# Kernel optimization log

Hardware: AMD Instinct MI355X
Metric: run time of the kernel (lower is better)

The kernel has to match this reference:

```python
import jax, jax.numpy as jnp
import numpy as np

EPS = 1e-05
DILATION = 1

def setup_inputs() -> dict:
    key = jax.random.key(0)
    k1, k2 = jax.random.split(key)
    B, T, D, K = 4, 4096, 2048, 4
    x = jax.random.normal(k1, (B, T, D), dtype=jnp.float32)
    norm_weight = jnp.ones((D,), dtype=jnp.float32)
    conv_weight = jax.random.normal(k2, (D, 1, K), dtype=jnp.float32) * (1.0 / np.sqrt(K))
    return {"x": x, "norm_weight": norm_weight, "conv_weight": conv_weight}

def reference(x, norm_weight, conv_weight):
    B, T, D = x.shape
    K = conv_weight.shape[-1]
    pad = (K - 1) * DILATION
    # RMSNorm over last dim
    ms = jnp.mean(jnp.square(x), axis=-1, keepdims=True)
    y = x * jax.lax.rsqrt(ms + EPS) * norm_weight
    # to channel-first [B, D, T]
    y = jnp.transpose(y, (0, 2, 1))
    # causal depthwise conv: left-pad (K-1)*dilation, valid conv == torch pad-both + slice[:T]
    y = jax.lax.conv_general_dilated(
        y, conv_weight,
        window_strides=(1,),
        padding=[(pad, 0)],
        rhs_dilation=(DILATION,),
        dimension_numbers=("NCH", "OIH", "NCH"),
        feature_group_count=D,
    )
    # SiLU then back to [B, T, D]
    y = y * jax.nn.sigmoid(y)
    return jnp.transpose(y, (0, 2, 1))
```

## Files before the change

kernel.cpp:

```cpp
#include <hip/hip_runtime.h>
#include <math.h>

#define D_DIM 2048
#define T_DIM 4096
#define TT    16
#define NT    (D_DIM / 4)
#define NW    (NT / 64)

typedef float vfloat4 __attribute__((ext_vector_type(4)));

__device__ __forceinline__ float row_partial(float4 v) {
    float p = v.x * v.x + v.y * v.y + v.z * v.z + v.w * v.w;
#pragma unroll
    for (int off = 32; off > 0; off >>= 1) p += __shfl_down(p, off, 64);
    return p;
}

__device__ __forceinline__ float inv_from(const float* sp) {
    float4 a = *(const float4*)sp;
    float4 b = *(const float4*)(sp + 4);
    float s = a.x + a.y + a.z + a.w + b.x + b.y + b.z + b.w;
    return rsqrtf(s * (1.0f / D_DIM) + 1e-5f);
}

__device__ __forceinline__ float silu(float v) {
    return v * __builtin_amdgcn_rcpf(1.f + __expf(-v));
}

__device__ __forceinline__ void nt_store4(float* p, float a, float b, float c, float d) {
    vfloat4 v = { a, b, c, d };
    __builtin_nontemporal_store(v, (vfloat4*)p);
}

__global__ __launch_bounds__(NT, 4) void fused_kernel(
    const float* __restrict__ x,
    const float* __restrict__ g,
    const float* __restrict__ w,
    float* __restrict__ out)
{
    const int b    = blockIdx.y;
    const int t0   = blockIdx.x * TT;
    const int tid  = threadIdx.x;
    const int d0   = tid * 4;
    const int lane = tid & 63;
    const int wid  = tid >> 6;

    __shared__ __align__(16) float part[TT + 3][NW];

    const float* xb = x   + (size_t)b * T_DIM * D_DIM + d0;
    float*       ob = out + (size_t)b * T_DIM * D_DIM + d0;

    float4 hv[3];
#pragma unroll
    for (int r = 0; r < 3; ++r) {
        const int t = t0 - 3 + r;
        hv[r] = (t >= 0) ? *(const float4*)(xb + (size_t)t * D_DIM)
                         : make_float4(0.f, 0.f, 0.f, 0.f);
    }
    float4 xv[TT];
#pragma unroll
    for (int i = 0; i < TT; ++i)
        xv[i] = *(const float4*)(xb + (size_t)(t0 + i) * D_DIM);

    const float4 gv = *(const float4*)(g + d0);
    float wgt[4][4];
#pragma unroll
    for (int j = 0; j < 4; ++j) {
        float4 wv = *(const float4*)(w + (size_t)(d0 + j) * 4);
        wgt[j][0] = wv.x; wgt[j][1] = wv.y; wgt[j][2] = wv.z; wgt[j][3] = wv.w;
    }

#pragma unroll
    for (int r = 0; r < 3; ++r) {
        float p = row_partial(hv[r]);
        if (lane == 0) part[r][wid] = p;
    }
#pragma unroll
    for (int i = 0; i < TT; ++i) {
        float p = row_partial(xv[i]);
        if (lane == 0) part[3 + i][wid] = p;
    }
    __syncthreads();

    float win[3][4];
#pragma unroll
    for (int r = 0; r < 3; ++r) {
        const float inv = inv_from(part[r]);
        win[r][0] = hv[r].x * inv * gv.x;
        win[r][1] = hv[r].y * inv * gv.y;
        win[r][2] = hv[r].z * inv * gv.z;
        win[r][3] = hv[r].w * inv * gv.w;
    }

#pragma unroll
    for (int i = 0; i < TT; ++i) {
        const float inv = inv_from(part[3 + i]);
        const float y0[4] = { xv[i].x * inv * gv.x, xv[i].y * inv * gv.y,
                              xv[i].z * inv * gv.z, xv[i].w * inv * gv.w };
        float o0[4];
#pragma unroll
        for (int j = 0; j < 4; ++j) {
            const float v = wgt[j][0] * win[0][j] + wgt[j][1] * win[1][j] +
                            wgt[j][2] * win[2][j] + wgt[j][3] * y0[j];
            o0[j] = silu(v);
        }
        nt_store4(ob + (size_t)(t0 + i) * D_DIM, o0[0], o0[1], o0[2], o0[3]);

#pragma unroll
        for (int j = 0; j < 4; ++j) {
            win[0][j] = win[1][j];
            win[1][j] = win[2][j];
            win[2][j] = y0[j];
        }
    }
}

extern "C" void kernel_launch(void* const* d_in, const int* in_sizes, int n_in,
                              void* d_out, int out_size, void* d_ws, size_t ws_size,
                              hipStream_t stream) {
    const float* x = (const float*)d_in[0];
    const float* g = (const float*)d_in[1];
    const float* w = (const float*)d_in[2];
    float* out = (float*)d_out;

    const int total = in_sizes[0];
    const int rows  = total / D_DIM;
    const int B     = rows / T_DIM;

    dim3 grid(T_DIM / TT, B);
    fused_kernel<<<grid, NT, 0, stream>>>(x, g, w, out);
}
```

Baseline: 238.6 us.

## Halve time tile and interleave row reductions across rows with sched barrier

Reduces the time tile from 16 to 8 rows per block, which doubles the block count and cuts per-thread register use. The per-row wavefront sum-of-squares reductions are interleaved so that shuffles for all rows run in one loop level, exposing instruction-level parallelism. A scheduling barrier stops the compiler from moving the loads past the reduction. The cost is a larger halo overhead, since 3 extra rows are now read per 8 rows instead of per 16.

Result: faster. 233.4 us (-2.2%).

```diff
diff --git a/kernel.cpp b/kernel.cpp
--- a/kernel.cpp
+++ b/kernel.cpp
@@ -3,17 +3,15 @@
 
 #define D_DIM 2048
 #define T_DIM 4096
-#define TT    16
+#define TT    8
 #define NT    (D_DIM / 4)
 #define NW    (NT / 64)
+#define NROW  (TT + 3)
 
 typedef float vfloat4 __attribute__((ext_vector_type(4)));
 
-__device__ __forceinline__ float row_partial(float4 v) {
-    float p = v.x * v.x + v.y * v.y + v.z * v.z + v.w * v.w;
-#pragma unroll
-    for (int off = 32; off > 0; off >>= 1) p += __shfl_down(p, off, 64);
-    return p;
+__device__ __forceinline__ float sumsq4(float4 v) {
+    return v.x * v.x + v.y * v.y + v.z * v.z + v.w * v.w;
 }
 
 __device__ __forceinline__ float inv_from(const float* sp) {
@@ -45,22 +43,21 @@
     const int lane = tid & 63;
     const int wid  = tid >> 6;
 
-    __shared__ __align__(16) float part[TT + 3][NW];
+    __shared__ __align__(16) float part[NROW][NW];
 
     const float* xb = x   + (size_t)b * T_DIM * D_DIM + d0;
     float*       ob = out + (size_t)b * T_DIM * D_DIM + d0;
 
-    float4 hv[3];
+    float4 rv[NROW];
 #pragma unroll
     for (int r = 0; r < 3; ++r) {
         const int t = t0 - 3 + r;
-        hv[r] = (t >= 0) ? *(const float4*)(xb + (size_t)t * D_DIM)
+        rv[r] = (t >= 0) ? *(const float4*)(xb + (size_t)t * D_DIM)
                          : make_float4(0.f, 0.f, 0.f, 0.f);
     }
-    float4 xv[TT];
 #pragma unroll
     for (int i = 0; i < TT; ++i)
-        xv[i] = *(const float4*)(xb + (size_t)(t0 + i) * D_DIM);
+        rv[3 + i] = *(const float4*)(xb + (size_t)(t0 + i) * D_DIM);
 
     const float4 gv = *(const float4*)(g + d0);
     float wgt[4][4];
@@ -70,15 +67,21 @@
         wgt[j][0] = wv.x; wgt[j][1] = wv.y; wgt[j][2] = wv.z; wgt[j][3] = wv.w;
     }
 
+    __builtin_amdgcn_sched_barrier(0);
+
+    float p[NROW];
 #pragma unroll
-    for (int r = 0; r < 3; ++r) {
-        float p = row_partial(hv[r]);
-        if (lane == 0) part[r][wid] = p;
+    for (int r = 0; r < NROW; ++r) p[r] = sumsq4(rv[r]);
+
+#pragma unroll
+    for (int off = 32; off > 0; off >>= 1) {
+#pragma unroll
+        for (int r = 0; r < NROW; ++r)
+            p[r] += __shfl_down(p[r], off, 64);
     }
+    if (lane == 0) {
 #pragma unroll
-    for (int i = 0; i < TT; ++i) {
-        float p = row_partial(xv[i]);
-        if (lane == 0) part[3 + i][wid] = p;
+        for (int r = 0; r < NROW; ++r) part[r][wid] = p[r];
     }
     __syncthreads();
 
@@ -86,17 +89,18 @@
 #pragma unroll
     for (int r = 0; r < 3; ++r) {
         const float inv = inv_from(part[r]);
-        win[r][0] = hv[r].x * inv * gv.x;
-        win[r][1] = hv[r].y * inv * gv.y;
-        win[r][2] = hv[r].z * inv * gv.z;
-        win[r][3] = hv[r].w * inv * gv.w;
+        win[r][0] = rv[r].x * inv * gv.x;
+        win[r][1] = rv[r].y * inv * gv.y;
+        win[r][2] = rv[r].z * inv * gv.z;
+        win[r][3] = rv[r].w * inv * gv.w;
     }
 
 #pragma unroll
     for (int i = 0; i < TT; ++i) {
         const float inv = inv_from(part[3 + i]);
-        const float y0[4] = { xv[i].x * inv * gv.x, xv[i].y * inv * gv.y,
-                              xv[i].z * inv * gv.z, xv[i].w * inv * gv.w };
+        const float4 xv = rv[3 + i];
+        const float y0[4] = { xv.x * inv * gv.x, xv.y * inv * gv.y,
+                              xv.z * inv * gv.z, xv.w * inv * gv.w };
         float o0[4];
 #pragma unroll
         for (int j = 0; j < 4; ++j) {
```

## Stage input rows in LDS via direct global-to-LDS loads with smaller time tiles

Applied to the files above, without the earlier changes.

Input rows, including the three causal halo rows, are loaded straight into shared memory using global_load_lds, and each wave computes one full row's RMS reduction. The time tile shrinks from 16 to 4 rows per block. This is meant to cut register pressure and cross-wave partial-sum traffic and to raise block-level parallelism. In exchange, halo rows are re-read far more often, which increases global read traffic, and the large LDS footprint limits occupancy.

New measurement: 231.9 us. 1.03x faster.

```diff
diff --git a/kernel.cpp b/kernel.cpp
--- a/kernel.cpp
+++ b/kernel.cpp
@@ -3,25 +3,15 @@
 
 #define D_DIM 2048
 #define T_DIM 4096
-#define TT    16
-#define NT    (D_DIM / 4)
-#define NW    (NT / 64)
+#define TT    4
+#define NT    512
+#define NW    8
+#define NROW  (TT + 3)
+#define ROW_F D_DIM
+#define AS1 __attribute__((address_space(1)))
+#define AS3 __attribute__((address_space(3)))
 
 typedef float vfloat4 __attribute__((ext_vector_type(4)));
-
-__device__ __forceinline__ float row_partial(float4 v) {
-    float p = v.x * v.x + v.y * v.y + v.z * v.z + v.w * v.w;
-#pragma unroll
-    for (int off = 32; off > 0; off >>= 1) p += __shfl_down(p, off, 64);
-    return p;
-}
-
-__device__ __forceinline__ float inv_from(const float* sp) {
-    float4 a = *(const float4*)sp;
-    float4 b = *(const float4*)(sp + 4);
-    float s = a.x + a.y + a.z + a.w + b.x + b.y + b.z + b.w;
-    return rsqrtf(s * (1.0f / D_DIM) + 1e-5f);
-}
 
 __device__ __forceinline__ float silu(float v) {
     return v * __builtin_amdgcn_rcpf(1.f + __expf(-v));
@@ -45,22 +35,23 @@
     const int lane = tid & 63;
     const int wid  = tid >> 6;
 
-    __shared__ __align__(16) float part[TT + 3][NW];
+    __shared__ __align__(16) float rows[NROW * ROW_F];
+    __shared__ __align__(16) float inv_s[NROW];
 
-    const float* xb = x   + (size_t)b * T_DIM * D_DIM + d0;
-    float*       ob = out + (size_t)b * T_DIM * D_DIM + d0;
+    const float* xb = x + (size_t)b * T_DIM * D_DIM;
 
-    float4 hv[3];
 #pragma unroll
-    for (int r = 0; r < 3; ++r) {
+    for (int r = 0; r < NROW; ++r) {
         const int t = t0 - 3 + r;
-        hv[r] = (t >= 0) ? *(const float4*)(xb + (size_t)t * D_DIM)
-                         : make_float4(0.f, 0.f, 0.f, 0.f);
+        float* ldst = rows + r * ROW_F + d0;
+        if (t >= 0) {
+            const float* gsrc = xb + (size_t)t * D_DIM + d0;
+            __builtin_amdgcn_global_load_lds((const AS1 void*)gsrc,
+                                             (AS3 void*)ldst, 16, 0, 0);
+        } else {
+            *(float4*)ldst = make_float4(0.f, 0.f, 0.f, 0.f);
+        }
     }
-    float4 xv[TT];
-#pragma unroll
-    for (int i = 0; i < TT; ++i)
-        xv[i] = *(const float4*)(xb + (size_t)(t0 + i) * D_DIM);
 
     const float4 gv = *(const float4*)(g + d0);
     float wgt[4][4];
@@ -70,48 +61,49 @@
         wgt[j][0] = wv.x; wgt[j][1] = wv.y; wgt[j][2] = wv.z; wgt[j][3] = wv.w;
     }
 
+    __syncthreads();
+
+    if (wid < NROW) {
+        const float* rp = rows + wid * ROW_F;
+        float p = 0.f;
 #pragma unroll
-    for (int r = 0; r < 3; ++r) {
-        float p = row_partial(hv[r]);
-        if (lane == 0) part[r][wid] = p;
-    }
+        for (int j = 0; j < 8; ++j) {
+            float4 v = *(const float4*)(rp + (j * 64 + lane) * 4);
+            p = fmaf(v.x, v.x, p); p = fmaf(v.y, v.y, p);
+            p = fmaf(v.z, v.z, p); p = fmaf(v.w, v.w, p);
+        }
 #pragma unroll
-    for (int i = 0; i < TT; ++i) {
-        float p = row_partial(xv[i]);
-        if (lane == 0) part[3 + i][wid] = p;
+        for (int off = 32; off > 0; off >>= 1) p += __shfl_down(p, off, 64);
+        if (lane == 0)
+            inv_s[wid] = rsqrtf(p * (1.0f / D_DIM) + 1e-5f);
     }
     __syncthreads();
 
-    float win[3][4];
+    float inv[NROW];
 #pragma unroll
-    for (int r = 0; r < 3; ++r) {
-        const float inv = inv_from(part[r]);
-        win[r][0] = hv[r].x * inv * gv.x;
-        win[r][1] = hv[r].y * inv * gv.y;
-        win[r][2] = hv[r].z * inv * gv.z;
-        win[r][3] = hv[r].w * inv * gv.w;
+    for (int r = 0; r < NROW; ++r) inv[r] = inv_s[r];
+
+    float n[NROW][4];
+#pragma unroll
+    for (int r = 0; r < NROW; ++r) {
+        float4 v = *(const float4*)(rows + r * ROW_F + d0);
+        n[r][0] = v.x * inv[r] * gv.x;
+        n[r][1] = v.y * inv[r] * gv.y;
+        n[r][2] = v.z * inv[r] * gv.z;
+        n[r][3] = v.w * inv[r] * gv.w;
     }
 
+    float* ob = out + (size_t)b * T_DIM * D_DIM + d0;
 #pragma unroll
     for (int i = 0; i < TT; ++i) {
-        const float inv = inv_from(part[3 + i]);
-        const float y0[4] = { xv[i].x * inv * gv.x, xv[i].y * inv * gv.y,
-                              xv[i].z * inv * gv.z, xv[i].w * inv * gv.w };
-        float o0[4];
+        float o[4];
 #pragma unroll
         for (int j = 0; j < 4; ++j) {
-            const float v = wgt[j][0] * win[0][j] + wgt[j][1] * win[1][j] +
-                            wgt[j][2] * win[2][j] + wgt[j][3] * y0[j];
-            o0[j] = silu(v);
+            const float v = wgt[j][0] * n[i][j]     + wgt[j][1] * n[i + 1][j] +
+                            wgt[j][2] * n[i + 2][j] + wgt[j][3] * n[i + 3][j];
+            o[j] = silu(v);
         }
-        nt_store4(ob + (size_t)(t0 + i) * D_DIM, o0[0], o0[1], o0[2], o0[3]);
-
-#pragma unroll
-        for (int j = 0; j < 4; ++j) {
-            win[0][j] = win[1][j];
-            win[1][j] = win[2][j];
-            win[2][j] = y0[j];
-        }
+        nt_store4(ob + (size_t)(t0 + i) * D_DIM, o[0], o[1], o[2], o[3]);
     }
 }
 
```
